# Optimization experiments

Hardware: AMD Instinct MI355X
Metric: run time of the kernel (lower is better)

## Reference

```python
import jax, jax.numpy as jnp
import numpy as np

EMBED_DIM = 1024
NUM_HEADS = 16
HEAD_DIM = EMBED_DIM // NUM_HEADS


def setup_inputs() -> dict:
    key = jax.random.key(0)
    k_x, k_wqkv, k_bqkv, k_wout, k_bout = jax.random.split(key, 5)
    scale = 1.0 / np.sqrt(EMBED_DIM)
    return {
        "x": jax.random.normal(k_x, (2, 2048, EMBED_DIM), dtype=jnp.float32),
        "W_qkv": jax.random.normal(k_wqkv, (3 * EMBED_DIM, EMBED_DIM), dtype=jnp.float32) * scale,
        "b_qkv": jax.random.normal(k_bqkv, (3 * EMBED_DIM,), dtype=jnp.float32) * scale,
        "W_out": jax.random.normal(k_wout, (EMBED_DIM, EMBED_DIM), dtype=jnp.float32) * scale,
        "b_out": jax.random.normal(k_bout, (EMBED_DIM,), dtype=jnp.float32) * scale,
    }


def reference(x, W_qkv, b_qkv, W_out, b_out):
    B, L, D = x.shape
    H, hd = NUM_HEADS, HEAD_DIM
    # fused QKV projection (torch Linear: x @ W.T + b)
    qkv = x @ W_qkv.T + b_qkv                      # [B, L, 3D]
    q, k, v = jnp.split(qkv, 3, axis=-1)           # each [B, L, D]
    # [B, L, D] -> [B, H, L, hd]
    q = q.reshape(B, L, H, hd).transpose(0, 2, 1, 3)
    k = k.reshape(B, L, H, hd).transpose(0, 2, 1, 3)
    v = v.reshape(B, L, H, hd).transpose(0, 2, 1, 3)
    attn = jnp.einsum("bhqd,bhkd->bhqk", q, k) / jnp.sqrt(jnp.float32(hd))
    attn = jax.nn.softmax(attn, axis=-1)           # [B, H, L, L]
    out = jnp.einsum("bhqk,bhkd->bhqd", attn, v)   # [B, H, L, hd]
    out = out.transpose(0, 2, 1, 3).reshape(B, L, D)
    return out @ W_out.T + b_out
```

## Files before the change

### kernel.cpp

```cpp
#include <hip/hip_runtime.h>
#include <hip/hip_bf16.h>

typedef __attribute__((ext_vector_type(8))) _Float16 f16x8;
typedef __attribute__((ext_vector_type(4))) _Float16 f16x4;
typedef __attribute__((ext_vector_type(2))) _Float16 f16x2;
typedef __attribute__((ext_vector_type(4))) float f32x4;
typedef __attribute__((ext_vector_type(16))) float f32x16;
typedef __attribute__((ext_vector_type(2))) __fp16 fp16v2;

__device__ __forceinline__ void gload16(const void* g, void* l) {
  __builtin_amdgcn_global_load_lds((const __attribute__((address_space(1))) void*)g,
                                   (__attribute__((address_space(3))) void*)l, 16, 0, 0);
}
__device__ __forceinline__ float fexp2(float x) {
#if __has_builtin(__builtin_amdgcn_exp2f)
  return __builtin_amdgcn_exp2f(x);
#else
  return exp2f(x);
#endif
}
__device__ __forceinline__ unsigned pk2(float a, float b) {
#if __has_builtin(__builtin_amdgcn_cvt_pkrtz)
  fp16v2 r = __builtin_amdgcn_cvt_pkrtz(a, b);
  return __builtin_bit_cast(unsigned, r);
#else
  f16x2 t;
  t[0] = (_Float16)a;
  t[1] = (_Float16)b;
  return __builtin_bit_cast(unsigned, t);
#endif
}

__global__ __launch_bounds__(256) void cast_all(const float* __restrict__ x,
                                                const float* __restrict__ wqkv,
                                                const float* __restrict__ wout,
                                                _Float16* __restrict__ xh,
                                                _Float16* __restrict__ wqkvh,
                                                _Float16* __restrict__ wouth) {
  const int i = (blockIdx.x * 256 + threadIdx.x) * 8;
  const float* s;
  _Float16* d;
  int off;
  if (i < 4194304) {
    s = x; d = xh; off = i;
  } else if (i < 7340032) {
    s = wqkv; d = wqkvh; off = i - 4194304;
  } else {
    s = wout; d = wouth; off = i - 7340032;
  }
  const float4 v0 = *reinterpret_cast<const float4*>(s + off);
  const float4 v1 = *reinterpret_cast<const float4*>(s + off + 4);
  f16x8 h;
  h[0] = (_Float16)v0.x; h[1] = (_Float16)v0.y; h[2] = (_Float16)v0.z; h[3] = (_Float16)v0.w;
  h[4] = (_Float16)v1.x; h[5] = (_Float16)v1.y; h[6] = (_Float16)v1.z; h[7] = (_Float16)v1.w;
  *reinterpret_cast<f16x8*>(d + off) = h;
}

__global__ __launch_bounds__(256) void gemm_qkv(
    const _Float16* __restrict__ A, const _Float16* __restrict__ Bm,
    const float* __restrict__ bias,
    _Float16* __restrict__ Qo, _Float16* __restrict__ Ko, _Float16* __restrict__ Vto,
    int Ndim, int Kdim) {
  __shared__ __align__(16) _Float16 As[2][128 * 32];
  __shared__ __align__(16) _Float16 Bs[2][128 * 32];
  const int tid = threadIdx.x, lane = tid & 63, wave = tid >> 6;
  const int wm = wave >> 1, wn = wave & 1;
  const int nwg = gridDim.x * gridDim.y;
  int bidl = blockIdx.y * gridDim.x + blockIdx.x;
  bidl = (bidl & 7) * (nwg >> 3) + (bidl >> 3);
  const int m0 = (bidl / gridDim.x) * 128, n0 = (bidl % gridDim.x) * 128;
  const int row = lane & 15, kk = (lane >> 4) * 8;

  const int r0 = tid >> 2, c0 = (tid & 3) * 8;
  const int r1 = (256 + tid) >> 2, c1 = ((256 + tid) & 3) * 8;
  const _Float16* a0 = A + (size_t)(m0 + r0) * Kdim + c0;
  const _Float16* a1 = A + (size_t)(m0 + r1) * Kdim + c1;
  const _Float16* b0 = Bm + (size_t)(n0 + r0) * Kdim + c0;
  const _Float16* b1 = Bm + (size_t)(n0 + r1) * Kdim + c1;

  f32x4 acc[4][4];
#pragma unroll
  for (int i = 0; i < 4; ++i)
#pragma unroll
    for (int j = 0; j < 4; ++j)
#pragma unroll
      for (int q = 0; q < 4; ++q) acc[i][j][q] = 0.f;

  auto STAGE = [&](int bufi, int k0) {
    char* dA = (char*)&As[bufi][0] + (wave * 64) * 16;
    char* dB = (char*)&Bs[bufi][0] + (wave * 64) * 16;
    gload16(a0 + k0, dA);
    gload16(a1 + k0, dA + 4096);
    gload16(b0 + k0, dB);
    gload16(b1 + k0, dB + 4096);
  };

  STAGE(0, 0);
  asm volatile("s_waitcnt vmcnt(0)" ::: "memory");
  __syncthreads();

  for (int k0 = 0; k0 < Kdim; k0 += 32) {
    const int cur = (k0 >> 5) & 1;
    if (k0 + 32 < Kdim) STAGE(cur ^ 1, k0 + 32);
    f16x8 af[4], bf[4];
#pragma unroll
    for (int i = 0; i < 4; ++i)
      af[i] = *reinterpret_cast<const f16x8*>(&As[cur][(wm * 64 + i * 16 + row) * 32 + kk]);
#pragma unroll
    for (int j = 0; j < 4; ++j)
      bf[j] = *reinterpret_cast<const f16x8*>(&Bs[cur][(wn * 64 + j * 16 + row) * 32 + kk]);
#pragma unroll
    for (int i = 0; i < 4; ++i)
#pragma unroll
      for (int j = 0; j < 4; ++j)
        acc[i][j] = __builtin_amdgcn_mfma_f32_16x16x32_f16(af[i], bf[j], acc[i][j], 0, 0, 0);
    asm volatile("s_waitcnt vmcnt(0)" ::: "memory");
    __syncthreads();
  }

#pragma unroll
  for (int i = 0; i < 4; ++i) {
#pragma unroll
    for (int j = 0; j < 4; ++j) {
#pragma unroll
      for (int q = 0; q < 4; ++q) {
        const int gm = m0 + wm * 64 + i * 16 + (lane >> 4) * 4 + q;
        const int gn = n0 + wn * 64 + j * 16 + row;
        const float c = acc[i][j][q] + bias[gn];
        const int b = gm >> 11, l = gm & 2047;
        const int part = gn >> 10, dD = gn & 1023;
        const int h = dD >> 6, dd = dD & 63;
        const int bh = b * 16 + h;
        if (part == 0)
          Qo[((size_t)bh * 2048 + l) * 64 + dd] = (_Float16)(c * 0.1803368801f);
        else if (part == 1)
          Ko[((size_t)bh * 2048 + l) * 64 + dd] = (_Float16)c;
        else
          Vto[((size_t)bh * 64 + dd) * 2048 + l] = (_Float16)c;
      }
    }
  }
}

__global__ __launch_bounds__(256) void gemm_out64(
    const _Float16* __restrict__ A, const _Float16* __restrict__ Bm,
    const float* __restrict__ bias, float* __restrict__ Cout, int Ndim, int Kdim) {
  __shared__ __align__(16) _Float16 As[2][128 * 32];
  __shared__ __align__(16) _Float16 Bs[2][64 * 32];
  const int tid = threadIdx.x, lane = tid & 63, wave = tid >> 6;
  const int wm = wave >> 1, wn = wave & 1;
  const int nwg = gridDim.x * gridDim.y;
  int bidl = blockIdx.y * gridDim.x + blockIdx.x;
  bidl = (bidl & 7) * (nwg >> 3) + (bidl >> 3);
  const int m0 = (bidl / gridDim.x) * 128, n0 = (bidl % gridDim.x) * 64;
  const int row = lane & 15, kk = (lane >> 4) * 8;

  const int r0 = tid >> 2, c0 = (tid & 3) * 8;
  const int r1 = (256 + tid) >> 2, c1 = ((256 + tid) & 3) * 8;
  const _Float16* a0 = A + (size_t)(m0 + r0) * Kdim + c0;
  const _Float16* a1 = A + (size_t)(m0 + r1) * Kdim + c1;
  const _Float16* b0 = Bm + (size_t)(n0 + r0) * Kdim + c0;

  f32x4 acc[4][2];
#pragma unroll
  for (int i = 0; i < 4; ++i)
#pragma unroll
    for (int j = 0; j < 2; ++j)
#pragma unroll
      for (int q = 0; q < 4; ++q) acc[i][j][q] = 0.f;

  auto STAGE = [&](int bufi, int k0) {
    char* dA = (char*)&As[bufi][0] + (wave * 64) * 16;
    char* dB = (char*)&Bs[bufi][0] + wave * 1024;
    gload16(a0 + k0, dA);
    gload16(a1 + k0, dA + 4096);
    gload16(b0 + k0, dB);
  };

  STAGE(0, 0);
  asm volatile("s_waitcnt vmcnt(0)" ::: "memory");
  __syncthreads();

  for (int k0 = 0; k0 < Kdim; k0 += 32) {
    const int cur = (k0 >> 5) & 1;
    if (k0 + 32 < Kdim) STAGE(cur ^ 1, k0 + 32);
    f16x8 af[4], bf[2];
#pragma unroll
    for (int i = 0; i < 4; ++i)
      af[i] = *reinterpret_cast<const f16x8*>(&As[cur][(wm * 64 + i * 16 + row) * 32 + kk]);
#pragma unroll
    for (int j = 0; j < 2; ++j)
      bf[j] = *reinterpret_cast<const f16x8*>(&Bs[cur][(wn * 32 + j * 16 + row) * 32 + kk]);
#pragma unroll
    for (int i = 0; i < 4; ++i)
#pragma unroll
      for (int j = 0; j < 2; ++j)
        acc[i][j] = __builtin_amdgcn_mfma_f32_16x16x32_f16(af[i], bf[j], acc[i][j], 0, 0, 0);
    asm volatile("s_waitcnt vmcnt(0)" ::: "memory");
    __syncthreads();
  }

#pragma unroll
  for (int i = 0; i < 4; ++i) {
#pragma unroll
    for (int j = 0; j < 2; ++j) {
#pragma unroll
      for (int q = 0; q < 4; ++q) {
        const int gm = m0 + wm * 64 + i * 16 + (lane >> 4) * 4 + q;
        const int gn = n0 + wn * 32 + j * 16 + row;
        Cout[(size_t)gm * Ndim + gn] = acc[i][j][q] + bias[gn];
      }
    }
  }
}

__global__ __launch_bounds__(256, 2) void attn_fwd(const _Float16* __restrict__ Qh,
                                                   const _Float16* __restrict__ Kh,
                                                   const _Float16* __restrict__ Vth,
                                                   _Float16* __restrict__ AO0,
                                                   _Float16* __restrict__ AO1,
                                                   float2* __restrict__ ml) {
  __shared__ __align__(16) uint4 KVs[2][1024];
  const int tid = threadIdx.x, lane = tid & 63, wave = tid >> 6;
  const int bid = blockIdx.x;
  const int bh = bid & 31;
  const int rest = bid >> 5;
  const int qb = rest >> 1, kvh = rest & 1;
  const int b = bh >> 4, h = bh & 15;
  const int q0 = qb * 128 + wave * 32;
  const _Float16* Qp = Qh + ((size_t)bh * 2048 + q0) * 64;
  const _Float16* Kp = Kh + (size_t)bh * 2048 * 64 + (size_t)kvh * 1024 * 64;
  const _Float16* Vp = Vth + (size_t)bh * 64 * 2048 + kvh * 1024;
  const int r31 = lane & 31, hl = lane >> 5, r7 = lane & 7;

  const int kr0 = tid >> 3, ks0 = (tid & 7) ^ (kr0 & 7);
  const int kr1 = (256 + tid) >> 3, ks1 = ((256 + tid) & 7) ^ (kr1 & 7);
  const _Float16* ksrc0 = Kp + (size_t)kr0 * 64 + ks0 * 8;
  const _Float16* ksrc1 = Kp + (size_t)kr1 * 64 + ks1 * 8;
  const _Float16* vsrc0 = Vp + (size_t)kr0 * 2048 + ks0 * 8;
  const _Float16* vsrc1 = Vp + (size_t)kr1 * 2048 + ks1 * 8;

  f16x8 qf[4];
#pragma unroll
  for (int kd = 0; kd < 4; ++kd)
    qf[kd] = *reinterpret_cast<const f16x8*>(&Qp[r31 * 64 + kd * 16 + hl * 8]);

  f32x16 o0, o1;
#pragma unroll
  for (int i = 0; i < 16; ++i) { o0[i] = 0.f; o1[i] = 0.f; }
  float mrun = 0.f, lsum = 0.f;

  auto STAGE = [&](uint4* base, int t) {
    gload16(ksrc0 + (size_t)t * 4096, base + wave * 64);
    gload16(ksrc1 + (size_t)t * 4096, base + 256 + wave * 64);
    gload16(vsrc0 + t * 64, base + 512 + wave * 64);
    gload16(vsrc1 + t * 64, base + 768 + wave * 64);
  };

  auto ITER = [&](int t, uint4* cur, uint4* nxt) {
    if (t < 15) STAGE(nxt, t + 1);
    const char* KB = (const char*)cur;
    const char* VB = (const char*)(cur + 512);

    const float negm = -mrun;
    f32x16 st[2];
    __builtin_amdgcn_s_setprio(1);
#pragma unroll
    for (int t32 = 0; t32 < 2; ++t32) {
#pragma unroll
      for (int i = 0; i < 16; ++i) st[t32][i] = negm;
#pragma unroll
      for (int kd = 0; kd < 4; ++kd) {
        const f16x8 kf = *reinterpret_cast<const f16x8*>(
            KB + (((t32 * 32 + r31) * 8 + ((kd * 2 + hl) ^ r7)) << 4));
        st[t32] = __builtin_amdgcn_mfma_f32_32x32x16_f16(kf, qf[kd], st[t32], 0, 0, 0);
      }
    }
    __builtin_amdgcn_s_setprio(0);

    f16x8 vf[2][2][2];
#pragma unroll
    for (int hh = 0; hh < 2; ++hh)
#pragma unroll
      for (int t32 = 0; t32 < 2; ++t32)
#pragma unroll
        for (int s = 0; s < 2; ++s)
          vf[hh][t32][s] = *reinterpret_cast<const f16x8*>(
              VB + (((hh * 32 + r31) * 8 + (((t32 * 2 + s) * 2 + hl) ^ r7)) << 4));

    float m16[16];
#pragma unroll
    for (int i = 0; i < 16; ++i) m16[i] = fmaxf(st[0][i], st[1][i]);
#pragma unroll
    for (int w = 8; w; w >>= 1)
#pragma unroll
      for (int i = 0; i < 8; ++i)
        if (i < w) m16[i] = fmaxf(m16[i], m16[i + w]);
    const float mt = m16[0];
    if (!__all(mt <= 11.f)) {
      const float mts = fmaxf(mt, __shfl_xor(mt, 32));
      const float d = fmaxf(mts, 0.f);
      const float al = fexp2(-d);
      lsum *= al;
#pragma unroll
      for (int i = 0; i < 16; ++i) { o0[i] *= al; o1[i] *= al; }
      mrun += d;
#pragma unroll
      for (int t32 = 0; t32 < 2; ++t32)
#pragma unroll
        for (int i = 0; i < 16; ++i) st[t32][i] -= d;
    }
    float pr[32];
#pragma unroll
    for (int i = 0; i < 16; ++i) pr[i] = fexp2(st[0][i]);
#pragma unroll
    for (int i = 0; i < 16; ++i) pr[16 + i] = fexp2(st[1][i]);
    float s16[16];
#pragma unroll
    for (int i = 0; i < 16; ++i) s16[i] = pr[i] + pr[16 + i];
#pragma unroll
    for (int w = 8; w; w >>= 1)
#pragma unroll
      for (int i = 0; i < 8; ++i)
        if (i < w) s16[i] += s16[i + w];
    lsum += s16[0];

    __builtin_amdgcn_s_setprio(1);
#pragma unroll
    for (int t32 = 0; t32 < 2; ++t32) {
#pragma unroll
      for (int s = 0; s < 2; ++s) {
        const int bi = t32 * 16 + s * 8;
        const unsigned Aw = pk2(pr[bi + 0], pr[bi + 1]);
        const unsigned A2 = pk2(pr[bi + 2], pr[bi + 3]);
        const unsigned Bw = pk2(pr[bi + 4], pr[bi + 5]);
        const unsigned B2 = pk2(pr[bi + 6], pr[bi + 7]);
        const unsigned r1 = __shfl_xor(hl ? Aw : Bw, 32);
        const unsigned r2 = __shfl_xor(hl ? A2 : B2, 32);
        union { unsigned u[4]; f16x8 v; } pf;
        pf.u[0] = hl ? r1 : Aw;
        pf.u[1] = hl ? r2 : A2;
        pf.u[2] = hl ? Bw : r1;
        pf.u[3] = hl ? B2 : r2;
        o0 = __builtin_amdgcn_mfma_f32_32x32x16_f16(vf[0][t32][s], pf.v, o0, 0, 0, 0);
        o1 = __builtin_amdgcn_mfma_f32_32x32x16_f16(vf[1][t32][s], pf.v, o1, 0, 0, 0);
      }
    }
    __builtin_amdgcn_s_setprio(0);

    if (t < 15) {
      asm volatile("s_waitcnt vmcnt(0)" ::: "memory");
      __syncthreads();
    }
  };

  STAGE(KVs[0], 0);
  asm volatile("s_waitcnt vmcnt(0)" ::: "memory");
  __syncthreads();

  for (int tt = 0; tt < 8; ++tt) {
    ITER(2 * tt, KVs[0], KVs[1]);
    ITER(2 * tt + 1, KVs[1], KVs[0]);
  }

  const float ltot = lsum + __shfl_xor(lsum, 32);
  const float inv = 1.f / ltot;
  _Float16* AOp = kvh ? AO1 : AO0;
  const size_t orow = (size_t)b * 2048 + q0 + r31;
#pragma unroll
  for (int hh = 0; hh < 2; ++hh) {
#pragma unroll
    for (int rr = 0; rr < 4; ++rr) {
      f16x4 c;
#pragma unroll
      for (int j = 0; j < 4; ++j)
        c[j] = (_Float16)((hh ? o1[rr * 4 + j] : o0[rr * 4 + j]) * inv);
      const int hd = 8 * rr + 4 * hl + 32 * hh;
      *reinterpret_cast<f16x4*>(&AOp[orow * 1024 + h * 64 + hd]) = c;
    }
  }
  if (hl == 0) ml[kvh * 65536 + bh * 2048 + q0 + r31] = make_float2(mrun, ltot);
}

__global__ __launch_bounds__(256) void attn_combine(const _Float16* __restrict__ AO1,
                                                    const float2* __restrict__ ml,
                                                    _Float16* __restrict__ AO0) {
  const int idx = (blockIdx.x * 256 + threadIdx.x) * 8;
  const int row = idx >> 10, col = idx & 1023;
  const int b = row >> 11, l = row & 2047, h = col >> 6;
  const int bh = b * 16 + h;
  const float2 m0 = ml[bh * 2048 + l];
  const float2 m1 = ml[65536 + bh * 2048 + l];
  const float ms = fmaxf(m0.x, m1.x);
  float w0 = m0.y * fexp2(m0.x - ms);
  float w1 = m1.y * fexp2(m1.x - ms);
  const float inv = 1.f / (w0 + w1);
  w0 *= inv;
  w1 *= inv;
  const f16x8 a = *reinterpret_cast<const f16x8*>(AO0 + idx);
  const f16x8 c = *reinterpret_cast<const f16x8*>(AO1 + idx);
  f16x8 r;
#pragma unroll
  for (int j = 0; j < 8; ++j) r[j] = (_Float16)(w0 * (float)a[j] + w1 * (float)c[j]);
  *reinterpret_cast<f16x8*>(AO0 + idx) = r;
}

extern "C" void kernel_launch(void* const* d_in, const int* in_sizes, int n_in, void* d_out,
                              int out_size, void* d_ws, size_t ws_size, hipStream_t stream) {
  const float* x = (const float*)d_in[0];
  const float* Wqkv = (const float*)d_in[1];
  const float* bqkv = (const float*)d_in[2];
  const float* Wout = (const float*)d_in[3];
  const float* bout = (const float*)d_in[4];
  float* out = (float*)d_out;

  char* ws = (char*)d_ws;
  _Float16* xh = (_Float16*)(ws);
  _Float16* wqkvh = (_Float16*)(ws + 8388608);
  _Float16* wouth = (_Float16*)(ws + 14680064);
  _Float16* Qh = (_Float16*)(ws + 16777216);
  _Float16* Kh = (_Float16*)(ws + 25165824);
  _Float16* Vth = (_Float16*)(ws + 33554432);
  _Float16* AO0 = (_Float16*)(ws + 41943040);
  _Float16* AO1 = (_Float16*)(ws);
  float2* ml = (float2*)(ws + 8388608);

  cast_all<<<4096, 256, 0, stream>>>(x, Wqkv, Wout, xh, wqkvh, wouth);
  gemm_qkv<<<dim3(24, 32), 256, 0, stream>>>(xh, wqkvh, bqkv, Qh, Kh, Vth, 3072, 1024);
  attn_fwd<<<1024, 256, 0, stream>>>(Qh, Kh, Vth, AO0, AO1, ml);
  attn_combine<<<2048, 256, 0, stream>>>(AO1, ml, AO0);
  gemm_out64<<<dim3(16, 32), 256, 0, stream>>>(AO0, wouth, bout, out, 1024, 1024);
}
```

Before: 132.4 us.

## Triple-buffer GEMMs, vectorize V-transpose stores, drop split-KV attention combine

Both GEMMs move from double to triple-buffered LDS staging with partial vmcnt waits and a single barrier per K step, so global loads for two steps ahead stay in flight. The QKV epilogue writes the transposed V tile with 4-wide vector stores along the sequence dimension instead of scalar stores. Attention no longer splits the KV range in two: each block walks all 2048 keys, and the combine kernel plus its max/sum buffer are removed. This halves the attention grid to 512 blocks, which may under-fill the GPU, and the larger LDS buffers may reduce GEMM occupancy.

```diff
diff --git a/kernel.cpp b/kernel.cpp
--- a/kernel.cpp
+++ b/kernel.cpp
@@ -61,8 +61,8 @@
     const float* __restrict__ bias,
     _Float16* __restrict__ Qo, _Float16* __restrict__ Ko, _Float16* __restrict__ Vto,
     int Ndim, int Kdim) {
-  __shared__ __align__(16) _Float16 As[2][128 * 32];
-  __shared__ __align__(16) _Float16 Bs[2][128 * 32];
+  __shared__ __align__(16) _Float16 As[3][4096];
+  __shared__ __align__(16) _Float16 Bs[3][4096];
   const int tid = threadIdx.x, lane = tid & 63, wave = tid >> 6;
   const int wm = wave >> 1, wn = wave & 1;
   const int nwg = gridDim.x * gridDim.y;
@@ -96,12 +96,17 @@
   };
 
   STAGE(0, 0);
-  asm volatile("s_waitcnt vmcnt(0)" ::: "memory");
-  __syncthreads();
-
-  for (int k0 = 0; k0 < Kdim; k0 += 32) {
-    const int cur = (k0 >> 5) & 1;
-    if (k0 + 32 < Kdim) STAGE(cur ^ 1, k0 + 32);
+  STAGE(1, 32);
+
+  const int NIT = Kdim >> 5;
+  for (int it = 0; it < NIT; ++it) {
+    if (it < NIT - 1)
+      asm volatile("s_waitcnt vmcnt(4)" ::: "memory");
+    else
+      asm volatile("s_waitcnt vmcnt(0)" ::: "memory");
+    __syncthreads();
+    if (it + 2 < NIT) STAGE((it + 2) % 3, (it + 2) * 32);
+    const int cur = it % 3;
     f16x8 af[4], bf[4];
 #pragma unroll
     for (int i = 0; i < 4; ++i)
@@ -114,29 +119,45 @@
 #pragma unroll
       for (int j = 0; j < 4; ++j)
         acc[i][j] = __builtin_amdgcn_mfma_f32_16x16x32_f16(af[i], bf[j], acc[i][j], 0, 0, 0);
-    asm volatile("s_waitcnt vmcnt(0)" ::: "memory");
-    __syncthreads();
-  }
-
-#pragma unroll
-  for (int i = 0; i < 4; ++i) {
-#pragma unroll
-    for (int j = 0; j < 4; ++j) {
-#pragma unroll
-      for (int q = 0; q < 4; ++q) {
-        const int gm = m0 + wm * 64 + i * 16 + (lane >> 4) * 4 + q;
+  }
+
+  const int part = n0 >> 10;
+  if (part == 2) {
+#pragma unroll
+    for (int i = 0; i < 4; ++i) {
+      const int gm = m0 + wm * 64 + i * 16 + (lane >> 4) * 4;
+      const int b = gm >> 11, l0 = gm & 2047;
+#pragma unroll
+      for (int j = 0; j < 4; ++j) {
         const int gn = n0 + wn * 64 + j * 16 + row;
-        const float c = acc[i][j][q] + bias[gn];
-        const int b = gm >> 11, l = gm & 2047;
-        const int part = gn >> 10, dD = gn & 1023;
+        const int dD = gn & 1023;
         const int h = dD >> 6, dd = dD & 63;
-        const int bh = b * 16 + h;
-        if (part == 0)
-          Qo[((size_t)bh * 2048 + l) * 64 + dd] = (_Float16)(c * 0.1803368801f);
-        else if (part == 1)
-          Ko[((size_t)bh * 2048 + l) * 64 + dd] = (_Float16)c;
-        else
-          Vto[((size_t)bh * 64 + dd) * 2048 + l] = (_Float16)c;
+        const float bb = bias[gn];
+        f16x4 v;
+#pragma unroll
+        for (int q = 0; q < 4; ++q) v[q] = (_Float16)(acc[i][j][q] + bb);
+        *reinterpret_cast<f16x4*>(&Vto[((size_t)(b * 16 + h) * 64 + dd) * 2048 + l0]) = v;
+      }
+    }
+  } else {
+#pragma unroll
+    for (int i = 0; i < 4; ++i) {
+#pragma unroll
+      for (int j = 0; j < 4; ++j) {
+#pragma unroll
+        for (int q = 0; q < 4; ++q) {
+          const int gm = m0 + wm * 64 + i * 16 + (lane >> 4) * 4 + q;
+          const int gn = n0 + wn * 64 + j * 16 + row;
+          const float c = acc[i][j][q] + bias[gn];
+          const int b = gm >> 11, l = gm & 2047;
+          const int dD = gn & 1023;
+          const int h = dD >> 6, dd = dD & 63;
+          const int bh = b * 16 + h;
+          if (part == 0)
+            Qo[((size_t)bh * 2048 + l) * 64 + dd] = (_Float16)(c * 0.1803368801f);
+          else
+            Ko[((size_t)bh * 2048 + l) * 64 + dd] = (_Float16)c;
+        }
       }
     }
   }
@@ -145,8 +166,8 @@
 __global__ __launch_bounds__(256) void gemm_out64(
     const _Float16* __restrict__ A, const _Float16* __restrict__ Bm,
     const float* __restrict__ bias, float* __restrict__ Cout, int Ndim, int Kdim) {
-  __shared__ __align__(16) _Float16 As[2][128 * 32];
-  __shared__ __align__(16) _Float16 Bs[2][64 * 32];
+  __shared__ __align__(16) _Float16 As[3][4096];
+  __shared__ __align__(16) _Float16 Bs[3][2048];
   const int tid = threadIdx.x, lane = tid & 63, wave = tid >> 6;
   const int wm = wave >> 1, wn = wave & 1;
   const int nwg = gridDim.x * gridDim.y;
@@ -178,12 +199,17 @@
   };
 
   STAGE(0, 0);
-  asm volatile("s_waitcnt vmcnt(0)" ::: "memory");
-  __syncthreads();
-
-  for (int k0 = 0; k0 < Kdim; k0 += 32) {
-    const int cur = (k0 >> 5) & 1;
-    if (k0 + 32 < Kdim) STAGE(cur ^ 1, k0 + 32);
+  STAGE(1, 32);
+
+  const int NIT = Kdim >> 5;
+  for (int it = 0; it < NIT; ++it) {
+    if (it < NIT - 1)
+      asm volatile("s_waitcnt vmcnt(3)" ::: "memory");
+    else
+      asm volatile("s_waitcnt vmcnt(0)" ::: "memory");
+    __syncthreads();
+    if (it + 2 < NIT) STAGE((it + 2) % 3, (it + 2) * 32);
+    const int cur = it % 3;
     f16x8 af[4], bf[2];
 #pragma unroll
     for (int i = 0; i < 4; ++i)
@@ -196,8 +222,6 @@
 #pragma unroll
       for (int j = 0; j < 2; ++j)
         acc[i][j] = __builtin_amdgcn_mfma_f32_16x16x32_f16(af[i], bf[j], acc[i][j], 0, 0, 0);
-    asm volatile("s_waitcnt vmcnt(0)" ::: "memory");
-    __syncthreads();
   }
 
 #pragma unroll
@@ -217,20 +241,16 @@
 __global__ __launch_bounds__(256, 2) void attn_fwd(const _Float16* __restrict__ Qh,
                                                    const _Float16* __restrict__ Kh,
                                                    const _Float16* __restrict__ Vth,
-                                                   _Float16* __restrict__ AO0,
-                                                   _Float16* __restrict__ AO1,
-                                                   float2* __restrict__ ml) {
+                                                   _Float16* __restrict__ AOh) {
   __shared__ __align__(16) uint4 KVs[2][1024];
   const int tid = threadIdx.x, lane = tid & 63, wave = tid >> 6;
   const int bid = blockIdx.x;
-  const int bh = bid & 31;
-  const int rest = bid >> 5;
-  const int qb = rest >> 1, kvh = rest & 1;
+  const int bh = bid & 31, qb = bid >> 5;
   const int b = bh >> 4, h = bh & 15;
   const int q0 = qb * 128 + wave * 32;
   const _Float16* Qp = Qh + ((size_t)bh * 2048 + q0) * 64;
-  const _Float16* Kp = Kh + (size_t)bh * 2048 * 64 + (size_t)kvh * 1024 * 64;
-  const _Float16* Vp = Vth + (size_t)bh * 64 * 2048 + kvh * 1024;
+  const _Float16* Kp = Kh + (size_t)bh * 2048 * 64;
+  const _Float16* Vp = Vth + (size_t)bh * 64 * 2048;
   const int r31 = lane & 31, hl = lane >> 5, r7 = lane & 7;
 
   const int kr0 = tid >> 3, ks0 = (tid & 7) ^ (kr0 & 7);
@@ -258,7 +278,7 @@
   };
 
   auto ITER = [&](int t, uint4* cur, uint4* nxt) {
-    if (t < 15) STAGE(nxt, t + 1);
+    if (t < 31) STAGE(nxt, t + 1);
     const char* KB = (const char*)cur;
     const char* VB = (const char*)(cur + 512);
 
@@ -348,7 +368,7 @@
     }
     __builtin_amdgcn_s_setprio(0);
 
-    if (t < 15) {
+    if (t < 31) {
       asm volatile("s_waitcnt vmcnt(0)" ::: "memory");
       __syncthreads();
     }
@@ -358,14 +378,13 @@
   asm volatile("s_waitcnt vmcnt(0)" ::: "memory");
   __syncthreads();
 
-  for (int tt = 0; tt < 8; ++tt) {
+  for (int tt = 0; tt < 16; ++tt) {
     ITER(2 * tt, KVs[0], KVs[1]);
     ITER(2 * tt + 1, KVs[1], KVs[0]);
   }
 
   const float ltot = lsum + __shfl_xor(lsum, 32);
   const float inv = 1.f / ltot;
-  _Float16* AOp = kvh ? AO1 : AO0;
   const size_t orow = (size_t)b * 2048 + q0 + r31;
 #pragma unroll
   for (int hh = 0; hh < 2; ++hh) {
@@ -376,33 +395,9 @@
       for (int j = 0; j < 4; ++j)
         c[j] = (_Float16)((hh ? o1[rr * 4 + j] : o0[rr * 4 + j]) * inv);
       const int hd = 8 * rr + 4 * hl + 32 * hh;
-      *reinterpret_cast<f16x4*>(&AOp[orow * 1024 + h * 64 + hd]) = c;
-    }
-  }
-  if (hl == 0) ml[kvh * 65536 + bh * 2048 + q0 + r31] = make_float2(mrun, ltot);
-}
-
-__global__ __launch_bounds__(256) void attn_combine(const _Float16* __restrict__ AO1,
-                                                    const float2* __restrict__ ml,
-                                                    _Float16* __restrict__ AO0) {
-  const int idx = (blockIdx.x * 256 + threadIdx.x) * 8;
-  const int row = idx >> 10, col = idx & 1023;
-  const int b = row >> 11, l = row & 2047, h = col >> 6;
-  const int bh = b * 16 + h;
-  const float2 m0 = ml[bh * 2048 + l];
-  const float2 m1 = ml[65536 + bh * 2048 + l];
-  const float ms = fmaxf(m0.x, m1.x);
-  float w0 = m0.y * fexp2(m0.x - ms);
-  float w1 = m1.y * fexp2(m1.x - ms);
-  const float inv = 1.f / (w0 + w1);
-  w0 *= inv;
-  w1 *= inv;
-  const f16x8 a = *reinterpret_cast<const f16x8*>(AO0 + idx);
-  const f16x8 c = *reinterpret_cast<const f16x8*>(AO1 + idx);
-  f16x8 r;
-#pragma unroll
-  for (int j = 0; j < 8; ++j) r[j] = (_Float16)(w0 * (float)a[j] + w1 * (float)c[j]);
-  *reinterpret_cast<f16x8*>(AO0 + idx) = r;
+      *reinterpret_cast<f16x4*>(&AOh[orow * 1024 + h * 64 + hd]) = c;
+    }
+  }
 }
 
 extern "C" void kernel_launch(void* const* d_in, const int* in_sizes, int n_in, void* d_out,
@@ -421,13 +416,10 @@
   _Float16* Qh = (_Float16*)(ws + 16777216);
   _Float16* Kh = (_Float16*)(ws + 25165824);
   _Float16* Vth = (_Float16*)(ws + 33554432);
-  _Float16* AO0 = (_Float16*)(ws + 41943040);
-  _Float16* AO1 = (_Float16*)(ws);
-  float2* ml = (float2*)(ws + 8388608);
+  _Float16* AOh = (_Float16*)(ws + 41943040);
 
   cast_all<<<4096, 256, 0, stream>>>(x, Wqkv, Wout, xh, wqkvh, wouth);
   gemm_qkv<<<dim3(24, 32), 256, 0, stream>>>(xh, wqkvh, bqkv, Qh, Kh, Vth, 3072, 1024);
-  attn_fwd<<<1024, 256, 0, stream>>>(Qh, Kh, Vth, AO0, AO1, ml);
-  attn_combine<<<2048, 256, 0, stream>>>(AO1, ml, AO0);
-  gemm_out64<<<dim3(16, 32), 256, 0, stream>>>(AO0, wouth, bout, out, 1024, 1024);
-}
+  attn_fwd<<<512, 256, 0, stream>>>(Qh, Kh, Vth, AOh);
+  gemm_out64<<<dim3(16, 32), 256, 0, stream>>>(AOh, wouth, bout, out, 1024, 1024);
+}
```

Result: no change. 134.1 us (+1.2%).
